# Kernel optimization log

Measured on AMD Instinct MI355X. Metric: run time of the kernel, lower is better.

Reference implementation:

```python
import jax, jax.numpy as jnp
import numpy as np

N = 512          # octave output grid resolution per cube side
M = 256          # input octave resolution
FACTOR = 0.5     # 2 ** (-factor), factor = 1
EPS = 1e-12


def make_cube_faces(n):
    # two triangles per quad on each of the 6 n x n side grids
    idx = np.arange(n * n).reshape(n, n)
    a = idx[:-1, :-1].ravel(); b = idx[:-1, 1:].ravel()
    c = idx[1:, :-1].ravel(); d = idx[1:, 1:].ravel()
    tris = np.concatenate([np.stack([a, b, c], 1), np.stack([b, d, c], 1)], 0)
    faces = np.concatenate([tris + s * n * n for s in range(6)], 0)
    return jnp.asarray(faces, jnp.int32)  # [F, 3]


def to_stacked(t):
    # [1, 6*m*m, 3] -> [6, 3, m, m]
    m = int(round((t.shape[1] // 6) ** 0.5))
    return t.reshape(6, m, m, 3).transpose(0, 3, 1, 2)


def to_vertices(s):
    # [6, 3, m, m] -> [1, 6*m*m, 3]
    return s.transpose(0, 2, 3, 1).reshape(1, -1, 3)


def resize_bilinear_ac(t, n):
    # bilinear, align_corners=True, square input [.., m, m] -> [.., n, n]
    m = t.shape[-1]
    coords = jnp.linspace(0.0, m - 1.0, n)
    i0 = jnp.clip(jnp.floor(coords).astype(jnp.int32), 0, m - 1)
    i1 = jnp.minimum(i0 + 1, m - 1)
    w = (coords - i0).astype(t.dtype)
    t = t[..., i0, :] * (1.0 - w)[:, None] + t[..., i1, :] * w[:, None]
    t = t[..., :, i0] * (1.0 - w) + t[..., :, i1] * w
    return t


def compute_face_normals(vert, faces):
    v = vert[0]                                  # [V, 3]
    v0, v1, v2 = v[faces[:, 0]], v[faces[:, 1]], v[faces[:, 2]]
    fn = jnp.cross(v1 - v0, v2 - v0)             # [F, 3]
    nrm = jnp.linalg.norm(fn, axis=-1, keepdims=True)
    return fn / jnp.maximum(nrm, EPS)


def compute_vertex_normals(vert, faces, face_normals):
    V = vert.shape[1]
    flat_idx = faces.reshape(-1)                          # [3F] f0v0,f0v1,f0v2,...
    rep = jnp.repeat(face_normals, 3, axis=0)             # [3F, 3]
    acc = jax.ops.segment_sum(rep, flat_idx, num_segments=V)  # scatter-add
    nrm = jnp.linalg.norm(acc, axis=-1, keepdims=True)
    return (acc / jnp.maximum(nrm, EPS))[None]            # [1, V, 3]


def get_vertex_normals(vert, faces):
    fn = compute_face_normals(vert, faces)
    normals = compute_vertex_normals(vert, faces, fn)
    stacked = to_stacked(normals)                         # [6, 3, n, n]
    sign = jnp.array([-1.0, 1.0, 1.0, -1.0, -1.0, 1.0], stacked.dtype)
    stacked = stacked * sign[:, None, None, None]
    return to_vertices(stacked)


def setup_inputs() -> dict:
    key = jax.random.key(0)
    k1, k2 = jax.random.split(key)
    vrt = jax.random.normal(k1, (1, 6 * M * M, 3), jnp.float32)
    nrm = jax.random.normal(k2, (1, 6 * M * M, 3), jnp.float32)
    ps = jnp.zeros((6, 1, N, N), jnp.float32)   # nn.Parameter(zeros * noise)
    faces = make_cube_faces(N)
    return {"vrt": vrt, "nrm": nrm, "ps": ps, "faces": faces}


def reference(vrt, nrm, ps, faces):
    vrt_s = resize_bilinear_ac(to_stacked(vrt), N)                 # [6,3,n,n]
    nrm_mag = jnp.linalg.norm(resize_bilinear_ac(to_stacked(nrm), N),
                              axis=1, keepdims=True)               # [6,1,n,n]
    stacked = vrt_s + FACTOR * jax.nn.sigmoid(ps) * nrm_mag
    vert = to_vertices(stacked)                                    # [1, V, 3]
    normals = get_vertex_normals(vert, faces)
    return vert, faces, normals
```

## Files before the change

### kernel.cpp

```cpp
#include <hip/hip_runtime.h>
#include <math.h>

#define NSZ 512
#define MSZ 256
#define NPIX (6 * NSZ * NSZ)
#define NQ   ((NSZ - 1) * (NSZ - 1))
#define NFACE (6 * 2 * NQ)
#define F3TOT (NFACE * 3)
#define TS 32
#define HS (TS + 2)
#define PS 20
#define NVB (6 * 16 * 16)
#define NFT12 (F3TOT / 12)
#define GRID (NVB * 3)

__device__ inline float fast_rcp(float x) {
    float r = __builtin_amdgcn_rcpf(x);
    return r * (2.0f - x * r);
}
__device__ inline float fast_rsqrt(float d) {
    float r = __builtin_amdgcn_rsqf(d);
    return r * (1.5f - 0.5f * d * r * r);
}
__device__ inline float fast_sigmoid(float x) {
    float e = __builtin_amdgcn_exp2f(-1.442695040888963f * x);
    return fast_rcp(1.0f + e);
}

__device__ inline void tri_acc4(const float4 A, const float4 B, const float4 C,
                                float& ax, float& ay, float& az) {
    float e1x = B.x - A.x, e1y = B.y - A.y, e1z = B.z - A.z;
    float e2x = C.x - A.x, e2y = C.y - A.y, e2z = C.z - A.z;
    float nx = e1y * e2z - e1z * e2y;
    float ny = e1z * e2x - e1x * e2z;
    float nz = e1x * e2y - e1y * e2x;
    float d  = fmaxf(nx * nx + ny * ny + nz * nz, 1e-24f);
    float r  = fast_rsqrt(d);
    ax += nx * r; ay += ny * r; az += nz * r;
}

__global__ __launch_bounds__(256) void k_all(const float* __restrict__ vrt,
                                             const float* __restrict__ nrm,
                                             const float* __restrict__ ps,
                                             float* __restrict__ out0,
                                             float* __restrict__ out1,
                                             float* __restrict__ out2) {
    __shared__ float4 spv[PS * PS];
    __shared__ float4 spn[PS * PS];
    __shared__ float4 sv4[HS * HS];

    int blk    = blockIdx.x;
    int triple = blk / 3;
    int pos    = blk - triple * 3;

    if (pos != 0) {
        int t = (triple * 2 + (pos - 1)) * 256 + threadIdx.x;
        if (t >= NFT12) return;
        unsigned ti = 4u * (unsigned)t;
        unsigned s  = ti / (2u * NQ);
        unsigned r1 = ti - s * (2u * NQ);
        unsigned ty = (r1 >= (unsigned)NQ) ? 1u : 0u;
        unsigned qi = r1 - ty * (unsigned)NQ;
        unsigned R  = qi / (NSZ - 1);
        unsigned Q  = qi - R * (NSZ - 1);
        unsigned sbase = s << 18;
        float v[12];
#pragma unroll
        for (int k = 0; k < 4; ++k) {
            unsigned a = sbase + (R << 9) + Q;
            v[3 * k + 0] = (float)(a + (ty ? 1u : 0u));
            v[3 * k + 1] = (float)(a + (ty ? (unsigned)(NSZ + 1) : 1u));
            v[3 * k + 2] = (float)(a + (unsigned)NSZ);
            Q++;
            if (Q == (unsigned)(NSZ - 1)) {
                Q = 0u; R++;
                if (R == (unsigned)(NSZ - 1)) {
                    R = 0u; ty++;
                    if (ty == 2u) { ty = 0u; sbase += (unsigned)(NSZ * NSZ); }
                }
            }
        }
        float4* o = (float4*)out1 + 3 * t;
        o[0] = make_float4(v[0], v[1], v[2],  v[3]);
        o[1] = make_float4(v[4], v[5], v[6],  v[7]);
        o[2] = make_float4(v[8], v[9], v[10], v[11]);
        return;
    }

    int f   = triple >> 8;
    int tl  = triple & 255;
    int tr  = (tl >> 4) * TS;
    int tq  = (tl & 15) * TS;
    int fbm = f * (MSZ * MSZ);
    int fbn = f * (NSZ * NSZ);

    int iy_base = max(0, ((tr - 1) * (MSZ - 1)) / (NSZ - 1));
    int ix_base = max(0, ((tq - 1) * (MSZ - 1)) / (NSZ - 1));

    for (int p = threadIdx.x; p < PS * PS; p += 256) {
        int r = p / PS, c = p - r * PS;
        int iy = min(iy_base + r, MSZ - 1);
        int ix = min(ix_base + c, MSZ - 1);
        int g  = (fbm + iy * MSZ + ix) * 3;
        spv[p] = make_float4(vrt[g], vrt[g + 1], vrt[g + 2], 0.0f);
        spn[p] = make_float4(nrm[g], nrm[g + 1], nrm[g + 2], 0.0f);
    }
    __syncthreads();

    const float scale = 255.0f / 511.0f;
    for (int p = threadIdx.x; p < HS * HS; p += 256) {
        int pr = p / HS, pq = p - pr * HS;
        int y = tr + pr - 1, x = tq + pq - 1;
        int yc = min(max(y, 0), NSZ - 1);
        int xc = min(max(x, 0), NSZ - 1);

        float cy = (float)yc * scale;
        float cx = (float)xc * scale;
        int iy0 = (int)floorf(cy); iy0 = iy0 < 0 ? 0 : (iy0 > MSZ - 1 ? MSZ - 1 : iy0);
        int ix0 = (int)floorf(cx); ix0 = ix0 < 0 ? 0 : (ix0 > MSZ - 1 ? MSZ - 1 : ix0);
        int iy1 = min(iy0 + 1, MSZ - 1);
        int ix1 = min(ix0 + 1, MSZ - 1);
        float wy = cy - (float)iy0;
        float wx = cx - (float)ix0;
        float w00 = (1.0f - wy) * (1.0f - wx);
        float w01 = (1.0f - wy) * wx;
        float w10 = wy * (1.0f - wx);
        float w11 = wy * wx;

        int l00 = (iy0 - iy_base) * PS + (ix0 - ix_base);
        int l01 = (iy0 - iy_base) * PS + (ix1 - ix_base);
        int l10 = (iy1 - iy_base) * PS + (ix0 - ix_base);
        int l11 = (iy1 - iy_base) * PS + (ix1 - ix_base);

        float4 a00 = spv[l00], a01 = spv[l01], a10 = spv[l10], a11 = spv[l11];
        float4 b00 = spn[l00], b01 = spn[l01], b10 = spn[l10], b11 = spn[l11];

        float vx = a00.x * w00 + a01.x * w01 + a10.x * w10 + a11.x * w11;
        float vy = a00.y * w00 + a01.y * w01 + a10.y * w10 + a11.y * w11;
        float vz = a00.z * w00 + a01.z * w01 + a10.z * w10 + a11.z * w11;
        float nx = b00.x * w00 + b01.x * w01 + b10.x * w10 + b11.x * w11;
        float ny = b00.y * w00 + b01.y * w01 + b10.y * w10 + b11.y * w11;
        float nz = b00.z * w00 + b01.z * w01 + b10.z * w10 + b11.z * w11;

        float mag = __builtin_amdgcn_sqrtf(nx * nx + ny * ny + nz * nz);
        float sig = fast_sigmoid(ps[fbn + yc * NSZ + xc]);
        float add = 0.5f * sig * mag;
        float ox = vx + add, oy = vy + add, oz = vz + add;

        sv4[p] = make_float4(ox, oy, oz, 0.0f);
        if (pr >= 1 && pr <= TS && pq >= 1 && pq <= TS) {
            int gi = (fbn + y * NSZ + x) * 3;
            out0[gi + 0] = ox;
            out0[gi + 1] = oy;
            out0[gi + 2] = oz;
        }
    }
    __syncthreads();

    float sg = (f == 1 || f == 2 || f == 5) ? 1.0f : -1.0f;
    for (int p = threadIdx.x; p < TS * TS; p += 256) {
        int r = p >> 5, q = p & 31;
        int lc = (r + 1) * HS + (q + 1);
        float4 C  = sv4[lc];
        float4 W  = sv4[lc - 1];
        float4 E  = sv4[lc + 1];
        float4 Nn = sv4[lc - HS];
        float4 S  = sv4[lc + HS];
        float4 NE = sv4[lc - HS + 1];
        float4 SW = sv4[lc + HS - 1];

        float ax = 0.0f, ay = 0.0f, az = 0.0f;
        tri_acc4(C,  E,  S,  ax, ay, az);
        tri_acc4(W,  C,  SW, ax, ay, az);
        tri_acc4(Nn, NE, C,  ax, ay, az);
        tri_acc4(C,  S,  SW, ax, ay, az);
        tri_acc4(Nn, C,  W,  ax, ay, az);
        tri_acc4(NE, E,  C,  ax, ay, az);

        float d  = fmaxf(ax * ax + ay * ay + az * az, 1e-24f);
        float rs = fast_rsqrt(d) * sg;
        int gi = (fbn + (tr + r) * NSZ + (tq + q)) * 3;
        out2[gi + 0] = ax * rs;
        out2[gi + 1] = ay * rs;
        out2[gi + 2] = az * rs;
    }
}

extern "C" void kernel_launch(void* const* d_in, const int* in_sizes, int n_in,
                              void* d_out, int out_size, void* d_ws, size_t ws_size,
                              hipStream_t stream) {
    const float* vrt = (const float*)d_in[0];
    const float* nrm = (const float*)d_in[1];
    const float* ps  = (const float*)d_in[2];

    float* out0 = (float*)d_out;
    float* out1 = out0 + (size_t)NPIX * 3;
    float* out2 = out1 + (size_t)NFACE * 3;

    k_all<<<GRID, 256, 0, stream>>>(vrt, nrm, ps, out0, out1, out2);
}
```

Baseline: 32.27 us.

## Precompute per-quad face normals in LDS, read bilinear inputs directly, split faces writer

Vertex-normal stage now computes the two triangle normals per quad once into shared memory and sums six cached normals per vertex, where before each vertex recomputed six cross products. The staged input patch is removed, so bilinear sampling reads vrt/nrm straight from global memory with fma lerps. The faces-index writer now has each thread emit a single float4 across 6 blocks per group instead of three float4s across 2 blocks. Together these add a barrier and more shared memory, trade LDS staging for redundant global loads, and change the grid shape.

```diff
diff --git a/kernel.cpp b/kernel.cpp
--- a/kernel.cpp
+++ b/kernel.cpp
@@ -4,15 +4,17 @@
 #define NSZ 512
 #define MSZ 256
 #define NPIX (6 * NSZ * NSZ)
-#define NQ   ((NSZ - 1) * (NSZ - 1))
-#define NFACE (6 * 2 * NQ)
-#define F3TOT (NFACE * 3)
+#define NQu  261121u
+#define NQ2u 522242u
+#define NFACE 3133452
+#define F3TOT 9400356
+#define NFT4  2350089
 #define TS 32
-#define HS (TS + 2)
-#define PS 20
-#define NVB (6 * 16 * 16)
-#define NFT12 (F3TOT / 12)
-#define GRID (NVB * 3)
+#define HS 34
+#define QS 33
+#define NVB 1536
+#define NFB 9216
+#define GRID (NVB * 7)
 
 __device__ inline float fast_rcp(float x) {
     float r = __builtin_amdgcn_rcpf(x);
@@ -26,17 +28,8 @@
     float e = __builtin_amdgcn_exp2f(-1.442695040888963f * x);
     return fast_rcp(1.0f + e);
 }
-
-__device__ inline void tri_acc4(const float4 A, const float4 B, const float4 C,
-                                float& ax, float& ay, float& az) {
-    float e1x = B.x - A.x, e1y = B.y - A.y, e1z = B.z - A.z;
-    float e2x = C.x - A.x, e2y = C.y - A.y, e2z = C.z - A.z;
-    float nx = e1y * e2z - e1z * e2y;
-    float ny = e1z * e2x - e1x * e2z;
-    float nz = e1x * e2y - e1y * e2x;
-    float d  = fmaxf(nx * nx + ny * ny + nz * nz, 1e-24f);
-    float r  = fast_rsqrt(d);
-    ax += nx * r; ay += ny * r; az += nz * r;
+__device__ inline float lerpf(float a, float b, float w) {
+    return __builtin_fmaf(w, b - a, a);
 }
 
 __global__ __launch_bounds__(256) void k_all(const float* __restrict__ vrt,
@@ -45,67 +38,55 @@
                                              float* __restrict__ out0,
                                              float* __restrict__ out1,
                                              float* __restrict__ out2) {
-    __shared__ float4 spv[PS * PS];
-    __shared__ float4 spn[PS * PS];
     __shared__ float4 sv4[HS * HS];
-
-    int blk    = blockIdx.x;
-    int triple = blk / 3;
-    int pos    = blk - triple * 3;
+    __shared__ float4 tnA[QS * QS];
+    __shared__ float4 tnB[QS * QS];
+
+    int blk = blockIdx.x;
+    int grp = blk / 7;
+    int pos = blk - grp * 7;
 
     if (pos != 0) {
-        int t = (triple * 2 + (pos - 1)) * 256 + threadIdx.x;
-        if (t >= NFT12) return;
-        unsigned ti = 4u * (unsigned)t;
-        unsigned s  = ti / (2u * NQ);
-        unsigned r1 = ti - s * (2u * NQ);
-        unsigned ty = (r1 >= (unsigned)NQ) ? 1u : 0u;
-        unsigned qi = r1 - ty * (unsigned)NQ;
-        unsigned R  = qi / (NSZ - 1);
-        unsigned Q  = qi - R * (NSZ - 1);
-        unsigned sbase = s << 18;
-        float v[12];
+        int t = (grp * 6 + (pos - 1)) * 256 + threadIdx.x;
+        if (t >= NFT4) return;
+        unsigned j   = 4u * (unsigned)t;
+        unsigned tri = j / 3u;
+        unsigned c0  = j - tri * 3u;
+        unsigned s   = tri / NQ2u;
+        unsigned r1  = tri - s * NQ2u;
+        unsigned ty  = (r1 >= NQu) ? 1u : 0u;
+        unsigned qi  = r1 - ty * NQu;
+        unsigned R   = qi / 511u;
+        unsigned Q   = qi - R * 511u;
+        unsigned a0  = (s << 18) + (R << 9) + Q;
+        unsigned Qn = Q + 1u, Rn = R, tyn = ty, sn = s;
+        if (Qn == 511u) {
+            Qn = 0u; Rn += 1u;
+            if (Rn == 511u) { Rn = 0u; tyn ^= 1u; if (tyn == 0u) sn += 1u; }
+        }
+        unsigned a1 = (sn << 18) + (Rn << 9) + Qn;
+
+        float v[4];
 #pragma unroll
-        for (int k = 0; k < 4; ++k) {
-            unsigned a = sbase + (R << 9) + Q;
-            v[3 * k + 0] = (float)(a + (ty ? 1u : 0u));
-            v[3 * k + 1] = (float)(a + (ty ? (unsigned)(NSZ + 1) : 1u));
-            v[3 * k + 2] = (float)(a + (unsigned)NSZ);
-            Q++;
-            if (Q == (unsigned)(NSZ - 1)) {
-                Q = 0u; R++;
-                if (R == (unsigned)(NSZ - 1)) {
-                    R = 0u; ty++;
-                    if (ty == 2u) { ty = 0u; sbase += (unsigned)(NSZ * NSZ); }
-                }
-            }
-        }
-        float4* o = (float4*)out1 + 3 * t;
-        o[0] = make_float4(v[0], v[1], v[2],  v[3]);
-        o[1] = make_float4(v[4], v[5], v[6],  v[7]);
-        o[2] = make_float4(v[8], v[9], v[10], v[11]);
+        for (int i = 0; i < 4; ++i) {
+            unsigned ci = c0 + (unsigned)i;
+            unsigned nx = (ci >= 3u) ? 1u : 0u;
+            ci -= nx * 3u;
+            unsigned a  = nx ? a1 : a0;
+            unsigned tt = nx ? tyn : ty;
+            unsigned sel = (ci == 2u) ? 512u : ((ci == 1u) ? (tt ? 513u : 1u) : tt);
+            v[i] = (float)(a + sel);
+        }
+        ((float4*)out1)[t] = make_float4(v[0], v[1], v[2], v[3]);
         return;
     }
 
-    int f   = triple >> 8;
-    int tl  = triple & 255;
+    int f   = grp >> 8;
+    int tl  = grp & 255;
     int tr  = (tl >> 4) * TS;
     int tq  = (tl & 15) * TS;
     int fbm = f * (MSZ * MSZ);
     int fbn = f * (NSZ * NSZ);
-
-    int iy_base = max(0, ((tr - 1) * (MSZ - 1)) / (NSZ - 1));
-    int ix_base = max(0, ((tq - 1) * (MSZ - 1)) / (NSZ - 1));
-
-    for (int p = threadIdx.x; p < PS * PS; p += 256) {
-        int r = p / PS, c = p - r * PS;
-        int iy = min(iy_base + r, MSZ - 1);
-        int ix = min(ix_base + c, MSZ - 1);
-        int g  = (fbm + iy * MSZ + ix) * 3;
-        spv[p] = make_float4(vrt[g], vrt[g + 1], vrt[g + 2], 0.0f);
-        spn[p] = make_float4(nrm[g], nrm[g + 1], nrm[g + 2], 0.0f);
-    }
-    __syncthreads();
 
     const float scale = 255.0f / 511.0f;
     for (int p = threadIdx.x; p < HS * HS; p += 256) {
@@ -116,31 +97,33 @@
 
         float cy = (float)yc * scale;
         float cx = (float)xc * scale;
-        int iy0 = (int)floorf(cy); iy0 = iy0 < 0 ? 0 : (iy0 > MSZ - 1 ? MSZ - 1 : iy0);
-        int ix0 = (int)floorf(cx); ix0 = ix0 < 0 ? 0 : (ix0 > MSZ - 1 ? MSZ - 1 : ix0);
-        int iy1 = min(iy0 + 1, MSZ - 1);
-        int ix1 = min(ix0 + 1, MSZ - 1);
+        int iy0 = min((int)cy, MSZ - 1);
+        int ix0 = min((int)cx, MSZ - 1);
         float wy = cy - (float)iy0;
         float wx = cx - (float)ix0;
-        float w00 = (1.0f - wy) * (1.0f - wx);
-        float w01 = (1.0f - wy) * wx;
-        float w10 = wy * (1.0f - wx);
-        float w11 = wy * wx;
-
-        int l00 = (iy0 - iy_base) * PS + (ix0 - ix_base);
-        int l01 = (iy0 - iy_base) * PS + (ix1 - ix_base);
-        int l10 = (iy1 - iy_base) * PS + (ix0 - ix_base);
-        int l11 = (iy1 - iy_base) * PS + (ix1 - ix_base);
-
-        float4 a00 = spv[l00], a01 = spv[l01], a10 = spv[l10], a11 = spv[l11];
-        float4 b00 = spn[l00], b01 = spn[l01], b10 = spn[l10], b11 = spn[l11];
-
-        float vx = a00.x * w00 + a01.x * w01 + a10.x * w10 + a11.x * w11;
-        float vy = a00.y * w00 + a01.y * w01 + a10.y * w10 + a11.y * w11;
-        float vz = a00.z * w00 + a01.z * w01 + a10.z * w10 + a11.z * w11;
-        float nx = b00.x * w00 + b01.x * w01 + b10.x * w10 + b11.x * w11;
-        float ny = b00.y * w00 + b01.y * w01 + b10.y * w10 + b11.y * w11;
-        float nz = b00.z * w00 + b01.z * w01 + b10.z * w10 + b11.z * w11;
+        int   iya = min(iy0, MSZ - 2);
+        int   ixa = min(ix0, MSZ - 2);
+        float wya = (iy0 < MSZ - 1) ? wy : 1.0f;
+        float wxa = (ix0 < MSZ - 1) ? wx : 1.0f;
+
+        int g0 = (fbm + iya * MSZ + ixa) * 3;
+        int g1 = g0 + MSZ * 3;
+
+        float va0 = vrt[g0], va1 = vrt[g0+1], va2 = vrt[g0+2];
+        float va3 = vrt[g0+3], va4 = vrt[g0+4], va5 = vrt[g0+5];
+        float vb0 = vrt[g1], vb1 = vrt[g1+1], vb2 = vrt[g1+2];
+        float vb3 = vrt[g1+3], vb4 = vrt[g1+4], vb5 = vrt[g1+5];
+        float na0 = nrm[g0], na1 = nrm[g0+1], na2 = nrm[g0+2];
+        float na3 = nrm[g0+3], na4 = nrm[g0+4], na5 = nrm[g0+5];
+        float nb0 = nrm[g1], nb1 = nrm[g1+1], nb2 = nrm[g1+2];
+        float nb3 = nrm[g1+3], nb4 = nrm[g1+4], nb5 = nrm[g1+5];
+
+        float vx = lerpf(lerpf(va0, va3, wxa), lerpf(vb0, vb3, wxa), wya);
+        float vy = lerpf(lerpf(va1, va4, wxa), lerpf(vb1, vb4, wxa), wya);
+        float vz = lerpf(lerpf(va2, va5, wxa), lerpf(vb2, vb5, wxa), wya);
+        float nx = lerpf(lerpf(na0, na3, wxa), lerpf(nb0, nb3, wxa), wya);
+        float ny = lerpf(lerpf(na1, na4, wxa), lerpf(nb1, nb4, wxa), wya);
+        float nz = lerpf(lerpf(na2, na5, wxa), lerpf(nb2, nb5, wxa), wya);
 
         float mag = __builtin_amdgcn_sqrtf(nx * nx + ny * ny + nz * nz);
         float sig = fast_sigmoid(ps[fbn + yc * NSZ + xc]);
@@ -157,25 +140,55 @@
     }
     __syncthreads();
 
+    for (int p = threadIdx.x; p < QS * QS; p += 256) {
+        int Ri = p / QS, Qi = p - Ri * QS;
+        int base = Ri * HS + Qi;
+        float4 A = sv4[base];
+        float4 B = sv4[base + 1];
+        float4 C = sv4[base + HS];
+        float4 D = sv4[base + HS + 1];
+
+        {
+            float e1x = B.x - A.x, e1y = B.y - A.y, e1z = B.z - A.z;
+            float e2x = C.x - A.x, e2y = C.y - A.y, e2z = C.z - A.z;
+            float cxp = e1y * e2z - e1z * e2y;
+            float cyp = e1z * e2x - e1x * e2z;
+            float czp = e1x * e2y - e1y * e2x;
+            float d = fmaxf(cxp * cxp + cyp * cyp + czp * czp, 1e-24f);
+            float r = fast_rsqrt(d);
+            tnA[p] = make_float4(cxp * r, cyp * r, czp * r, 0.0f);
+        }
+        {
+            float e1x = D.x - B.x, e1y = D.y - B.y, e1z = D.z - B.z;
+            float e2x = C.x - B.x, e2y = C.y - B.y, e2z = C.z - B.z;
+            float cxp = e1y * e2z - e1z * e2y;
+            float cyp = e1z * e2x - e1x * e2z;
+            float czp = e1x * e2y - e1y * e2x;
+            float d = fmaxf(cxp * cxp + cyp * cyp + czp * czp, 1e-24f);
+            float r = fast_rsqrt(d);
+            tnB[p] = make_float4(cxp * r, cyp * r, czp * r, 0.0f);
+        }
+    }
+    __syncthreads();
+
     float sg = (f == 1 || f == 2 || f == 5) ? 1.0f : -1.0f;
     for (int p = threadIdx.x; p < TS * TS; p += 256) {
         int r = p >> 5, q = p & 31;
-        int lc = (r + 1) * HS + (q + 1);
-        float4 C  = sv4[lc];
-        float4 W  = sv4[lc - 1];
-        float4 E  = sv4[lc + 1];
-        float4 Nn = sv4[lc - HS];
-        float4 S  = sv4[lc + HS];
-        float4 NE = sv4[lc - HS + 1];
-        float4 SW = sv4[lc + HS - 1];
-
-        float ax = 0.0f, ay = 0.0f, az = 0.0f;
-        tri_acc4(C,  E,  S,  ax, ay, az);
-        tri_acc4(W,  C,  SW, ax, ay, az);
-        tri_acc4(Nn, NE, C,  ax, ay, az);
-        tri_acc4(C,  S,  SW, ax, ay, az);
-        tri_acc4(Nn, C,  W,  ax, ay, az);
-        tri_acc4(NE, E,  C,  ax, ay, az);
+        int q00 = r * QS + q;
+        int q01 = q00 + 1;
+        int q10 = q00 + QS;
+        int q11 = q10 + 1;
+
+        float4 t0 = tnA[q11];
+        float4 t1 = tnA[q10];
+        float4 t2 = tnA[q01];
+        float4 t3 = tnB[q10];
+        float4 t4 = tnB[q00];
+        float4 t5 = tnB[q01];
+
+        float ax = t0.x + t1.x + t2.x + t3.x + t4.x + t5.x;
+        float ay = t0.y + t1.y + t2.y + t3.y + t4.y + t5.y;
+        float az = t0.z + t1.z + t2.z + t3.z + t4.z + t5.z;
 
         float d  = fmaxf(ax * ax + ay * ay + az * az, 1e-24f);
         float rs = fast_rsqrt(d) * sg;
@@ -195,7 +208,7 @@
 
     float* out0 = (float*)d_out;
     float* out1 = out0 + (size_t)NPIX * 3;
-    float* out2 = out1 + (size_t)NFACE * 3;
+    float* out2 = out1 + (size_t)F3TOT;
 
     k_all<<<GRID, 256, 0, stream>>>(vrt, nrm, ps, out0, out1, out2);
 }
```

After: 34.26 us. 1.06x slower.
